# Performance work log

Hardware: AMD Instinct MI355X
Metric: run time of the kernel (lower is better)

The kernel has to match this reference:

```python
import jax, jax.numpy as jnp
import numpy as np

B, T, V = 16, 512, 8000
BLANK = 0
LSM = 0.1
W_SOFT = 0.5


def setup_inputs() -> dict:
    rng = np.random.default_rng(0)
    key = jax.random.key(0)
    k1, k2 = jax.random.split(key)

    align = rng.integers(1, V, size=(B, T))
    align = np.where(rng.random((B, T)) < 0.6, BLANK, align)
    align[:, 0] = rng.integers(1, V, size=B)  # guarantee >=1 non-blank run
    xlens = rng.integers(T // 2, T + 1, size=B)
    frame_mask = np.arange(T)[None, :] < xlens[:, None]
    align = np.where(frame_mask, align, BLANK)  # zero out padding frames

    # derive consistent ylens = number of non-blank runs within xlen
    nonblank = align != BLANK
    shifted = np.concatenate([np.full((B, 1), BLANK, dtype=align.dtype), align[:, :-1]], axis=1)
    ylens = (nonblank & (align != shifted)).sum(axis=1)

    ys = rng.integers(1, V, size=(B, T))  # hard labels, L = T (safe upper bound)
    logits = jax.random.normal(k1, (B, T, V), dtype=jnp.float32)
    soft_labels = jax.nn.softmax(jax.random.normal(k2, (B, T, V), dtype=jnp.float32), axis=-1)

    return {
        "logits": logits,
        "ys": jnp.asarray(ys, dtype=jnp.int32),
        "soft_labels": soft_labels,
        "aligns": jnp.asarray(align, dtype=jnp.int32),
        "xlens": jnp.asarray(xlens, dtype=jnp.int32),
        "ylens": jnp.asarray(ylens, dtype=jnp.int32),
    }


def reference(logits, ys, soft_labels, aligns, xlens, ylens):
    # position='all': every non-blank frame t maps to its run index (label_id).
    frame_mask = jnp.arange(T)[None, :] < xlens[:, None]          # [B,T]
    a = jnp.where(frame_mask, aligns, BLANK)
    nonblank = a != BLANK                                          # = label_exists
    shifted = jnp.pad(a[:, :-1], ((0, 0), (1, 0)), constant_values=BLANK)
    run_start = nonblank & (a != shifted)
    label_id = jnp.cumsum(run_start.astype(jnp.int32), axis=1) - 1  # [B,T]
    lm = jnp.maximum(label_id, 0)                                  # clamp; masked where blank

    logp = jax.nn.log_softmax(logits, axis=-1)                     # [B,T,V]
    n_exists = nonblank.sum(axis=1).astype(logp.dtype)             # [B]

    # soft part: sum_v soft_labels[b, lm[b,t], v] * logp[b,t,v]
    soft_g = jnp.take_along_axis(soft_labels, lm[:, :, None], axis=1)  # [B,T,V]
    frame_soft = jnp.sum(soft_g * logp, axis=-1)                   # [B,T]
    loss_soft = jnp.sum(jnp.where(nonblank, frame_soft, 0.0), axis=1) / n_exists

    # hard part with label smoothing: (1-e)*logp[y] + e/(V-1)*(sum_v logp - logp[y])
    y_t = jnp.take_along_axis(ys, lm, axis=1)                      # [B,T]
    logp_y = jnp.take_along_axis(logp, y_t[:, :, None], axis=2)[..., 0]
    sum_lp = jnp.sum(logp, axis=-1)
    frame_hard = (1.0 - LSM) * logp_y + (LSM / (V - 1)) * (sum_lp - logp_y)
    loss_hard = jnp.sum(jnp.where(nonblank, frame_hard, 0.0), axis=1) / n_exists

    per_b = W_SOFT * loss_soft + (1.0 - W_SOFT) * loss_hard
    return -jnp.mean(per_b)
```

## Files before the change

### kernel.cpp

```cpp
#include <hip/hip_runtime.h>
#include <math.h>

#define BB 16
#define TT 512
#define VV 8000
#define BLANK 0
#define LSM 0.1f
#define W_SOFT 0.5f
#define BLOCK 256

__global__ __launch_bounds__(TT) void meta_kernel(
    const int* __restrict__ aligns,
    const int* __restrict__ xlens,
    int* __restrict__ meta,
    float* __restrict__ inv_nexists,
    float* __restrict__ out) {
  int b = blockIdx.x;
  int t = threadIdx.x;
  if (b == 0 && t == 0) out[0] = 0.0f;

  __shared__ int s[TT];
  int xlen = xlens[b];
  int a  = (t < xlen) ? aligns[b * TT + t] : BLANK;
  int ap = BLANK;
  if (t > 0) ap = ((t - 1) < xlen) ? aligns[b * TT + t - 1] : BLANK;
  int nonblank = (a != BLANK) ? 1 : 0;
  int runstart = (nonblank && (a != ap)) ? 1 : 0;

  s[t] = runstart;
  __syncthreads();
  for (int off = 1; off < TT; off <<= 1) {
    int v = (t >= off) ? s[t - off] : 0;
    __syncthreads();
    s[t] += v;
    __syncthreads();
  }
  int label_id = s[t] - 1;
  meta[b * TT + t] = nonblank ? label_id : -1;
  __syncthreads();

  s[t] = nonblank;
  __syncthreads();
  for (int off = TT / 2; off > 0; off >>= 1) {
    if (t < off) s[t] += s[t + off];
    __syncthreads();
  }
  if (t == 0) inv_nexists[b] = 1.0f / (float)s[0];
}

__global__ __launch_bounds__(BLOCK) void frame_kernel(
    const float* __restrict__ logits,
    const int* __restrict__ ys,
    const float* __restrict__ soft,
    const int* __restrict__ meta,
    const float* __restrict__ inv_nexists,
    float* __restrict__ out) {
  int idx = blockIdx.x;
  int lm = meta[idx];
  if (lm < 0) return;
  int b = idx / TT;

  __shared__ float red[8];

  const float* xrow = logits + (size_t)idx * VV;
  const float* srow = soft + ((size_t)(b * TT + lm)) * VV;
  int tid = threadIdx.x;
  int wid = tid >> 6;

  int y = ys[b * TT + lm];
  float xy = xrow[y];

  float4 xr[8];
  float tmax = -INFINITY, tsum = 0.0f;
#pragma unroll
  for (int k = 0; k < 8; ++k) {
    int i = tid * 4 + k * (BLOCK * 4);
    if (i < VV) {
      float4 x = *(const float4*)(xrow + i);
      xr[k] = x;
      tmax = fmaxf(tmax, fmaxf(fmaxf(x.x, x.y), fmaxf(x.z, x.w)));
      tsum += (x.x + x.y) + (x.z + x.w);
    } else {
      xr[k] = make_float4(-INFINITY, -INFINITY, -INFINITY, -INFINITY);
    }
  }
  for (int off = 32; off > 0; off >>= 1) {
    tmax = fmaxf(tmax, __shfl_xor(tmax, off));
    tsum += __shfl_xor(tsum, off);
  }
  if ((tid & 63) == 0) { red[wid] = tmax; red[4 + wid] = tsum; }
  __syncthreads();
  float bmax = fmaxf(fmaxf(red[0], red[1]), fmaxf(red[2], red[3]));
  float bsum = (red[4] + red[5]) + (red[6] + red[7]);
  __syncthreads();

  float tse = 0.0f;
#pragma unroll
  for (int k = 0; k < 8; ++k) {
    tse += __expf(xr[k].x - bmax) + __expf(xr[k].y - bmax) +
           __expf(xr[k].z - bmax) + __expf(xr[k].w - bmax);
  }
  for (int off = 32; off > 0; off >>= 1) tse += __shfl_xor(tse, off);
  if ((tid & 63) == 0) red[wid] = tse;
  __syncthreads();
  float sumexp = (red[0] + red[1]) + (red[2] + red[3]);
  float C = bmax + logf(sumexp);
  __syncthreads();

  float tdot = 0.0f;
#pragma unroll
  for (int k = 0; k < 8; ++k) {
    int i = tid * 4 + k * (BLOCK * 4);
    if (i < VV) {
      float4 sv = *(const float4*)(srow + i);
      float4 x = xr[k];
      tdot += sv.x * (x.x - C) + sv.y * (x.y - C) +
              sv.z * (x.z - C) + sv.w * (x.w - C);
    }
  }
  for (int off = 32; off > 0; off >>= 1) tdot += __shfl_xor(tdot, off);
  if ((tid & 63) == 0) red[wid] = tdot;
  __syncthreads();

  if (tid == 0) {
    float dot = (red[0] + red[1]) + (red[2] + red[3]);
    float logp_y = xy - C;
    float sum_lp = bsum - (float)VV * C;
    float frame_hard = (1.0f - LSM) * logp_y +
                       (LSM / (float)(VV - 1)) * (sum_lp - logp_y);
    float val = W_SOFT * dot + (1.0f - W_SOFT) * frame_hard;
    atomicAdd(out, -val * inv_nexists[b] * (1.0f / (float)BB));
  }
}

extern "C" void kernel_launch(void* const* d_in, const int* in_sizes, int n_in,
                              void* d_out, int out_size, void* d_ws, size_t ws_size,
                              hipStream_t stream) {
  const float* logits = (const float*)d_in[0];
  const int*   ys     = (const int*)d_in[1];
  const float* soft   = (const float*)d_in[2];
  const int*   aligns = (const int*)d_in[3];
  const int*   xlens  = (const int*)d_in[4];

  int*   meta  = (int*)d_ws;
  float* inv_n = (float*)((char*)d_ws + (size_t)BB * TT * sizeof(int));
  float* out   = (float*)d_out;

  meta_kernel<<<BB, TT, 0, stream>>>(aligns, xlens, meta, inv_n, out);
  frame_kernel<<<BB * TT, BLOCK, 0, stream>>>(logits, ys, soft, meta, inv_n, out);
}
```

Before: 439.4 us.

## Prefetch soft-label row with logits and use wave shuffles for scan

```diff
diff --git a/kernel.cpp b/kernel.cpp
--- a/kernel.cpp
+++ b/kernel.cpp
@@ -19,7 +19,6 @@
   int t = threadIdx.x;
   if (b == 0 && t == 0) out[0] = 0.0f;
 
-  __shared__ int s[TT];
   int xlen = xlens[b];
   int a  = (t < xlen) ? aligns[b * TT + t] : BLANK;
   int ap = BLANK;
@@ -27,25 +26,35 @@
   int nonblank = (a != BLANK) ? 1 : 0;
   int runstart = (nonblank && (a != ap)) ? 1 : 0;
 
-  s[t] = runstart;
-  __syncthreads();
-  for (int off = 1; off < TT; off <<= 1) {
-    int v = (t >= off) ? s[t - off] : 0;
-    __syncthreads();
-    s[t] += v;
-    __syncthreads();
+  int lane = t & 63;
+  int w = t >> 6;
+
+  int val = runstart;
+#pragma unroll
+  for (int off = 1; off < 64; off <<= 1) {
+    int v = __shfl_up(val, off);
+    if (lane >= off) val += v;
   }
-  int label_id = s[t] - 1;
-  meta[b * TT + t] = nonblank ? label_id : -1;
+  int cnt = nonblank;
+#pragma unroll
+  for (int off = 32; off > 0; off >>= 1) cnt += __shfl_xor(cnt, off);
+
+  __shared__ int wsum[8], wcnt[8];
+  if (lane == 63) wsum[w] = val;
+  if (lane == 0)  wcnt[w] = cnt;
   __syncthreads();
 
-  s[t] = nonblank;
-  __syncthreads();
-  for (int off = TT / 2; off > 0; off >>= 1) {
-    if (t < off) s[t] += s[t + off];
-    __syncthreads();
+  int base = 0;
+#pragma unroll
+  for (int i = 0; i < 8; ++i) if (i < w) base += wsum[i];
+  meta[b * TT + t] = nonblank ? (base + val - 1) : -1;
+
+  if (t == 0) {
+    int total = 0;
+#pragma unroll
+    for (int i = 0; i < 8; ++i) total += wcnt[i];
+    inv_nexists[b] = 1.0f / (float)total;
   }
-  if (t == 0) inv_nexists[b] = 1.0f / (float)s[0];
 }
 
 __global__ __launch_bounds__(BLOCK) void frame_kernel(
@@ -58,7 +67,7 @@
   int idx = blockIdx.x;
   int lm = meta[idx];
   if (lm < 0) return;
-  int b = idx / TT;
+  int b = idx >> 9;
 
   __shared__ float red[8];
 
@@ -67,21 +76,30 @@
   int tid = threadIdx.x;
   int wid = tid >> 6;
 
+  float4 xr[8], sr[8];
+#pragma unroll
+  for (int k = 0; k < 8; ++k) {
+    int i = tid * 4 + k * (BLOCK * 4);
+    if (i < VV) {
+      xr[k] = *(const float4*)(xrow + i);
+      sr[k] = *(const float4*)(srow + i);
+    } else {
+      xr[k] = make_float4(-INFINITY, -INFINITY, -INFINITY, -INFINITY);
+      sr[k] = make_float4(0.0f, 0.0f, 0.0f, 0.0f);
+    }
+  }
   int y = ys[b * TT + lm];
   float xy = xrow[y];
+  __builtin_amdgcn_sched_barrier(0);
 
-  float4 xr[8];
   float tmax = -INFINITY, tsum = 0.0f;
 #pragma unroll
   for (int k = 0; k < 8; ++k) {
     int i = tid * 4 + k * (BLOCK * 4);
     if (i < VV) {
-      float4 x = *(const float4*)(xrow + i);
-      xr[k] = x;
+      float4 x = xr[k];
       tmax = fmaxf(tmax, fmaxf(fmaxf(x.x, x.y), fmaxf(x.z, x.w)));
       tsum += (x.x + x.y) + (x.z + x.w);
-    } else {
-      xr[k] = make_float4(-INFINITY, -INFINITY, -INFINITY, -INFINITY);
     }
   }
   for (int off = 32; off > 0; off >>= 1) {
@@ -112,7 +130,7 @@
   for (int k = 0; k < 8; ++k) {
     int i = tid * 4 + k * (BLOCK * 4);
     if (i < VV) {
-      float4 sv = *(const float4*)(srow + i);
+      float4 sv = sr[k];
       float4 x = xr[k];
       tdot += sv.x * (x.x - C) + sv.y * (x.y - C) +
               sv.z * (x.z - C) + sv.w * (x.w - C);
```

New measurement: 432.2 us. Within noise of the previous version (-1.6%).
